# Kernel tuning notes

Measured on AMD Instinct MI355X. Metric: run time of the kernel, lower is better.

Reference implementation:

```python
import jax, jax.numpy as jnp
import numpy as np

NUM_ITEMS = 100000
D_SEM = 768
D_PROMPT = 384
D_MODEL = 2048
B, T = 64, 200


def setup_inputs() -> dict:
    key = jax.random.key(0)
    k_ids, k_len, k_sem, k_vp, k_w = jax.random.split(key, 5)
    ids = jax.random.randint(k_ids, (B, T), 0, NUM_ITEMS, dtype=jnp.int64 if jax.config.jax_enable_x64 else jnp.int32)
    lengths = jax.random.randint(k_len, (B,), 1, T + 1, dtype=ids.dtype)
    # positions beyond each sequence length are padding (-1), as produced by the dataloader
    pos = jnp.arange(T, dtype=ids.dtype)[None, :]
    ids = jnp.where(pos < lengths[:, None], ids, -1)
    E_sem = jax.random.normal(k_sem, (NUM_ITEMS, D_SEM), dtype=jnp.float32)
    v_prompt = 0.02 * jax.random.normal(k_vp, (NUM_ITEMS, D_PROMPT), dtype=jnp.float32)
    # nn.Linear weight: [out_features, in_features]
    proj_w = jax.random.normal(k_w, (D_MODEL, D_SEM + D_PROMPT), dtype=jnp.float32) * (1.0 / np.sqrt(D_SEM + D_PROMPT))
    return {"batch_item_ids_padded": ids, "batch_lengths": lengths,
            "E_sem": E_sem, "v_prompt": v_prompt, "proj_w": proj_w}


def reference(batch_item_ids_padded, batch_lengths, E_sem, v_prompt, proj_w):
    """Vectorized build_inputs_embeds: gather + concat + projection, masked.
    Returns (embeds [B,T,d_model], amask [B,T], tok_item_ids [B,T])."""
    ids = batch_item_ids_padded
    num_items = E_sem.shape[0]
    valid = (ids >= 0) & (ids < num_items)            # [B,T]
    safe = jnp.where(valid, ids, 0)                   # clamp for safe gather
    sem = E_sem[safe]                                 # [B,T,d_sem]
    vp = v_prompt[safe]                               # [B,T,d_prompt]
    cat = jnp.concatenate([sem, vp], axis=-1)         # [B,T,d_sem+d_prompt]
    tok = jnp.einsum('btk,dk->btd', cat, proj_w)      # [B,T,d_model]
    embeds = jnp.where(valid[..., None], tok, jnp.zeros((), tok.dtype))
    amask = valid.astype(jnp.int32)
    tok_item_ids = jnp.where(valid, ids, -1)
    return embeds, amask, tok_item_ids
```

## Files before the change

### kernel.cpp

```cpp
#include <hip/hip_runtime.h>
#include <stdint.h>

constexpr int BB = 64, TT = 200;
constexpr int M  = BB * TT;
constexpr int DSEM = 768, DPR = 384;
constexpr int Kd = DSEM + DPR;
constexpr int Nd = 2048;
constexpr int NUM_ITEMS = 100000;

typedef short bf16x8 __attribute__((ext_vector_type(8)));
typedef float f32x4  __attribute__((ext_vector_type(4)));

__device__ __forceinline__ unsigned short f2bf(float f) {
  union { float f; uint32_t u; } v; v.f = f;
  uint32_t u = v.u;
  u += 0x7fffu + ((u >> 16) & 1u);
  return (unsigned short)(u >> 16);
}

__global__ void wconv_kernel(const float* __restrict__ w, unsigned short* __restrict__ wb) {
  int g = blockIdx.x * blockDim.x + threadIdx.x;
  int e = g * 4;
  float4 v = *(const float4*)(w + e);
  ushort4 o;
  o.x = f2bf(v.x); o.y = f2bf(v.y); o.z = f2bf(v.z); o.w = f2bf(v.w);
  *(ushort4*)(wb + e) = o;
}

__global__ void gather_kernel(const int* __restrict__ ids,
                              const float* __restrict__ Esem,
                              const float* __restrict__ vpr,
                              unsigned short* __restrict__ A) {
  unsigned g = blockIdx.x * blockDim.x + threadIdx.x;
  unsigned row = g / 288u;
  unsigned col = (g - row * 288u) * 4u;
  int id = ids[row];
  bool valid = (id >= 0) && (id < NUM_ITEMS);
  int safe = valid ? id : 0;
  const float* src = (col < (unsigned)DSEM)
                       ? (Esem + (size_t)safe * DSEM + col)
                       : (vpr  + (size_t)safe * DPR  + (col - DSEM));
  float4 v = *(const float4*)src;
  if (!valid) { v.x = 0.f; v.y = 0.f; v.z = 0.f; v.w = 0.f; }
  ushort4 o;
  o.x = f2bf(v.x); o.y = f2bf(v.y); o.z = f2bf(v.z); o.w = f2bf(v.w);
  *(ushort4*)(A + (size_t)row * Kd + col) = o;
}

__global__ void mask_kernel(const int* __restrict__ ids,
                            float* __restrict__ amask, float* __restrict__ tok) {
  int i = blockIdx.x * blockDim.x + threadIdx.x;
  if (i >= M) return;
  int id = ids[i];
  bool valid = (id >= 0) && (id < NUM_ITEMS);
  amask[i] = valid ? 1.0f : 0.0f;
  tok[i]   = valid ? (float)id : -1.0f;
}

__device__ __forceinline__ void async16(const void* gsrc, void* ldst) {
  __builtin_amdgcn_global_load_lds(
      (const __attribute__((address_space(1))) unsigned int*)gsrc,
      (__attribute__((address_space(3))) unsigned int*)ldst,
      16, 0, 0);
}

__global__ __launch_bounds__(256) void gemm_kernel(const unsigned short* __restrict__ A,
                                                   const unsigned short* __restrict__ Wb,
                                                   float* __restrict__ C) {
  __shared__ unsigned short lds_a[128 * 32];
  __shared__ unsigned short lds_b[128 * 32];

  const int tid  = threadIdx.x;
  const int lane = tid & 63;
  const int wave = tid >> 6;
  const int wm = wave >> 1, wn = wave & 1;
  const int quad = lane >> 4, lm = lane & 15;
  const int m0 = blockIdx.x * 128;
  const int n0 = blockIdx.y * 128;

  const int srow = tid >> 2;
  const int scol = (tid & 3) * 8;

  f32x4 acc[4][4];
#pragma unroll
  for (int i = 0; i < 4; ++i)
#pragma unroll
    for (int j = 0; j < 4; ++j) acc[i][j] = (f32x4){0.f, 0.f, 0.f, 0.f};

  for (int kt = 0; kt < Kd / 32; ++kt) {
    const int k0 = kt * 32;
#pragma unroll
    for (int r = 0; r < 2; ++r) {
      const unsigned short* ga = A + (size_t)(m0 + r * 64 + srow) * Kd + k0 + scol;
      async16(ga, lds_a + (size_t)(r * 256 + wave * 64) * 8);
      const unsigned short* gb = Wb + (size_t)(n0 + r * 64 + srow) * Kd + k0 + scol;
      async16(gb, lds_b + (size_t)(r * 256 + wave * 64) * 8);
    }
    __syncthreads();

    bf16x8 af[4], bf[4];
#pragma unroll
    for (int mi = 0; mi < 4; ++mi)
      af[mi] = *(const bf16x8*)(lds_a + (wm * 64 + mi * 16 + lm) * 32 + quad * 8);
#pragma unroll
    for (int ni = 0; ni < 4; ++ni)
      bf[ni] = *(const bf16x8*)(lds_b + (wn * 64 + ni * 16 + lm) * 32 + quad * 8);
#pragma unroll
    for (int mi = 0; mi < 4; ++mi)
#pragma unroll
      for (int ni = 0; ni < 4; ++ni)
        acc[mi][ni] = __builtin_amdgcn_mfma_f32_16x16x32_bf16(af[mi], bf[ni], acc[mi][ni], 0, 0, 0);
    __syncthreads();
  }

#pragma unroll
  for (int mi = 0; mi < 4; ++mi) {
#pragma unroll
    for (int ni = 0; ni < 4; ++ni) {
      const int row = m0 + wm * 64 + mi * 16 + quad * 4;
      const int col = n0 + wn * 64 + ni * 16 + lm;
#pragma unroll
      for (int i = 0; i < 4; ++i)
        C[(size_t)(row + i) * Nd + col] = acc[mi][ni][i];
    }
  }
}

extern "C" void kernel_launch(void* const* d_in, const int* in_sizes, int n_in,
                              void* d_out, int out_size, void* d_ws, size_t ws_size,
                              hipStream_t stream) {
  const int*   ids  = (const int*)d_in[0];
  const float* Esem = (const float*)d_in[2];
  const float* vpr  = (const float*)d_in[3];
  const float* pw   = (const float*)d_in[4];

  float* out_emb   = (float*)d_out;
  float* out_amask = out_emb + (size_t)M * Nd;
  float* out_tok   = out_amask + M;

  unsigned short* A  = (unsigned short*)d_ws;
  unsigned short* Wb = A + (size_t)M * Kd;

  gather_kernel<<<(M * Kd / 4) / 256, 256, 0, stream>>>(ids, Esem, vpr, A);
  wconv_kernel<<<(Nd * Kd / 4) / 256, 256, 0, stream>>>(pw, Wb);
  mask_kernel<<<(M + 255) / 256, 256, 0, stream>>>(ids, out_amask, out_tok);
  gemm_kernel<<<dim3(M / 128, Nd / 128), 256, 0, stream>>>(A, Wb, out_emb);
}
```

Baseline: 547.1 us.

## Double GEMM K-tile with XOR-swizzled LDS and merge prep kernels into one launch

The GEMM K-tile grows from 32 to 64, which halves the number of barrier pairs per block, and LDS chunks are XOR-swizzled so fragment reads avoid bank conflicts. The gather, weight-conversion and mask kernels are merged into one prep kernel that branches on block index, saving two launches. LDS per block doubles, which may reduce occupancy. There is still no double buffering, so loads and MFMA work do not overlap.

```diff
diff --git a/kernel.cpp b/kernel.cpp
--- a/kernel.cpp
+++ b/kernel.cpp
@@ -7,6 +7,11 @@
 constexpr int Kd = DSEM + DPR;
 constexpr int Nd = 2048;
 constexpr int NUM_ITEMS = 100000;
+constexpr int BK = 64;
+
+constexpr int GATHER_BLOCKS = (M * Kd / 4) / 256;
+constexpr int WCONV_BLOCKS  = (Nd * Kd / 4) / 256;
+constexpr int MASK_BLOCKS   = (M + 255) / 256;
 
 typedef short bf16x8 __attribute__((ext_vector_type(8)));
 typedef float f32x4  __attribute__((ext_vector_type(4)));
@@ -18,43 +23,47 @@
   return (unsigned short)(u >> 16);
 }
 
-__global__ void wconv_kernel(const float* __restrict__ w, unsigned short* __restrict__ wb) {
-  int g = blockIdx.x * blockDim.x + threadIdx.x;
-  int e = g * 4;
-  float4 v = *(const float4*)(w + e);
-  ushort4 o;
-  o.x = f2bf(v.x); o.y = f2bf(v.y); o.z = f2bf(v.z); o.w = f2bf(v.w);
-  *(ushort4*)(wb + e) = o;
-}
-
-__global__ void gather_kernel(const int* __restrict__ ids,
-                              const float* __restrict__ Esem,
-                              const float* __restrict__ vpr,
-                              unsigned short* __restrict__ A) {
-  unsigned g = blockIdx.x * blockDim.x + threadIdx.x;
-  unsigned row = g / 288u;
-  unsigned col = (g - row * 288u) * 4u;
-  int id = ids[row];
-  bool valid = (id >= 0) && (id < NUM_ITEMS);
-  int safe = valid ? id : 0;
-  const float* src = (col < (unsigned)DSEM)
-                       ? (Esem + (size_t)safe * DSEM + col)
-                       : (vpr  + (size_t)safe * DPR  + (col - DSEM));
-  float4 v = *(const float4*)src;
-  if (!valid) { v.x = 0.f; v.y = 0.f; v.z = 0.f; v.w = 0.f; }
-  ushort4 o;
-  o.x = f2bf(v.x); o.y = f2bf(v.y); o.z = f2bf(v.z); o.w = f2bf(v.w);
-  *(ushort4*)(A + (size_t)row * Kd + col) = o;
-}
-
-__global__ void mask_kernel(const int* __restrict__ ids,
-                            float* __restrict__ amask, float* __restrict__ tok) {
-  int i = blockIdx.x * blockDim.x + threadIdx.x;
-  if (i >= M) return;
-  int id = ids[i];
-  bool valid = (id >= 0) && (id < NUM_ITEMS);
-  amask[i] = valid ? 1.0f : 0.0f;
-  tok[i]   = valid ? (float)id : -1.0f;
+__global__ void prep_kernel(const int* __restrict__ ids,
+                            const float* __restrict__ Esem,
+                            const float* __restrict__ vpr,
+                            const float* __restrict__ pw,
+                            unsigned short* __restrict__ A,
+                            unsigned short* __restrict__ Wb,
+                            float* __restrict__ amask,
+                            float* __restrict__ tok) {
+  const int b = blockIdx.x;
+  const int tid = threadIdx.x;
+  if (b < GATHER_BLOCKS) {
+    unsigned g = (unsigned)b * 256u + tid;
+    unsigned row = g / 288u;
+    unsigned col = (g - row * 288u) * 4u;
+    int id = ids[row];
+    bool valid = (id >= 0) && (id < NUM_ITEMS);
+    int safe = valid ? id : 0;
+    const float* src = (col < (unsigned)DSEM)
+                         ? (Esem + (size_t)safe * DSEM + col)
+                         : (vpr  + (size_t)safe * DPR  + (col - DSEM));
+    float4 v = *(const float4*)src;
+    if (!valid) { v.x = 0.f; v.y = 0.f; v.z = 0.f; v.w = 0.f; }
+    ushort4 o;
+    o.x = f2bf(v.x); o.y = f2bf(v.y); o.z = f2bf(v.z); o.w = f2bf(v.w);
+    *(ushort4*)(A + (size_t)row * Kd + col) = o;
+  } else if (b < GATHER_BLOCKS + WCONV_BLOCKS) {
+    int g = (b - GATHER_BLOCKS) * 256 + tid;
+    int e = g * 4;
+    float4 v = *(const float4*)(pw + e);
+    ushort4 o;
+    o.x = f2bf(v.x); o.y = f2bf(v.y); o.z = f2bf(v.z); o.w = f2bf(v.w);
+    *(ushort4*)(Wb + e) = o;
+  } else {
+    int i = (b - GATHER_BLOCKS - WCONV_BLOCKS) * 256 + tid;
+    if (i < M) {
+      int id = ids[i];
+      bool valid = (id >= 0) && (id < NUM_ITEMS);
+      amask[i] = valid ? 1.0f : 0.0f;
+      tok[i]   = valid ? (float)id : -1.0f;
+    }
+  }
 }
 
 __device__ __forceinline__ void async16(const void* gsrc, void* ldst) {
@@ -67,8 +76,8 @@
 __global__ __launch_bounds__(256) void gemm_kernel(const unsigned short* __restrict__ A,
                                                    const unsigned short* __restrict__ Wb,
                                                    float* __restrict__ C) {
-  __shared__ unsigned short lds_a[128 * 32];
-  __shared__ unsigned short lds_b[128 * 32];
+  __shared__ unsigned short lds_a[128 * BK];
+  __shared__ unsigned short lds_b[128 * BK];
 
   const int tid  = threadIdx.x;
   const int lane = tid & 63;
@@ -78,8 +87,8 @@
   const int m0 = blockIdx.x * 128;
   const int n0 = blockIdx.y * 128;
 
-  const int srow = tid >> 2;
-  const int scol = (tid & 3) * 8;
+  const int srow   = tid >> 3;
+  const int schunk = tid & 7;
 
   f32x4 acc[4][4];
 #pragma unroll
@@ -87,29 +96,38 @@
 #pragma unroll
     for (int j = 0; j < 4; ++j) acc[i][j] = (f32x4){0.f, 0.f, 0.f, 0.f};
 
-  for (int kt = 0; kt < Kd / 32; ++kt) {
-    const int k0 = kt * 32;
+  for (int kt = 0; kt < Kd / BK; ++kt) {
+    const int k0 = kt * BK;
 #pragma unroll
-    for (int r = 0; r < 2; ++r) {
-      const unsigned short* ga = A + (size_t)(m0 + r * 64 + srow) * Kd + k0 + scol;
+    for (int r = 0; r < 4; ++r) {
+      const int row = r * 32 + srow;
+      const int gch = schunk ^ (row & 7);
+      const unsigned short* ga = A + (size_t)(m0 + row) * Kd + k0 + gch * 8;
       async16(ga, lds_a + (size_t)(r * 256 + wave * 64) * 8);
-      const unsigned short* gb = Wb + (size_t)(n0 + r * 64 + srow) * Kd + k0 + scol;
+      const unsigned short* gb = Wb + (size_t)(n0 + row) * Kd + k0 + gch * 8;
       async16(gb, lds_b + (size_t)(r * 256 + wave * 64) * 8);
     }
     __syncthreads();
 
-    bf16x8 af[4], bf[4];
 #pragma unroll
-    for (int mi = 0; mi < 4; ++mi)
-      af[mi] = *(const bf16x8*)(lds_a + (wm * 64 + mi * 16 + lm) * 32 + quad * 8);
+    for (int h = 0; h < 2; ++h) {
+      bf16x8 af[4], bfr[4];
 #pragma unroll
-    for (int ni = 0; ni < 4; ++ni)
-      bf[ni] = *(const bf16x8*)(lds_b + (wn * 64 + ni * 16 + lm) * 32 + quad * 8);
+      for (int mi = 0; mi < 4; ++mi) {
+        const int row = wm * 64 + mi * 16 + lm;
+        af[mi] = *(const bf16x8*)(lds_a + row * BK + ((h * 4 + quad) ^ (row & 7)) * 8);
+      }
 #pragma unroll
-    for (int mi = 0; mi < 4; ++mi)
+      for (int ni = 0; ni < 4; ++ni) {
+        const int row = wn * 64 + ni * 16 + lm;
+        bfr[ni] = *(const bf16x8*)(lds_b + row * BK + ((h * 4 + quad) ^ (row & 7)) * 8);
+      }
 #pragma unroll
-      for (int ni = 0; ni < 4; ++ni)
-        acc[mi][ni] = __builtin_amdgcn_mfma_f32_16x16x32_bf16(af[mi], bf[ni], acc[mi][ni], 0, 0, 0);
+      for (int mi = 0; mi < 4; ++mi)
+#pragma unroll
+        for (int ni = 0; ni < 4; ++ni)
+          acc[mi][ni] = __builtin_amdgcn_mfma_f32_16x16x32_bf16(af[mi], bfr[ni], acc[mi][ni], 0, 0, 0);
+    }
     __syncthreads();
   }
 
@@ -141,8 +159,7 @@
   unsigned short* A  = (unsigned short*)d_ws;
   unsigned short* Wb = A + (size_t)M * Kd;
 
-  gather_kernel<<<(M * Kd / 4) / 256, 256, 0, stream>>>(ids, Esem, vpr, A);
-  wconv_kernel<<<(Nd * Kd / 4) / 256, 256, 0, stream>>>(pw, Wb);
-  mask_kernel<<<(M + 255) / 256, 256, 0, stream>>>(ids, out_amask, out_tok);
+  prep_kernel<<<GATHER_BLOCKS + WCONV_BLOCKS + MASK_BLOCKS, 256, 0, stream>>>(
+      ids, Esem, vpr, pw, A, Wb, out_amask, out_tok);
   gemm_kernel<<<dim3(M / 128, Nd / 128), 256, 0, stream>>>(A, Wb, out_emb);
 }
```

Result: faster. 526.3 us (-3.8%).
